# Kernel optimization log

Hardware: AMD Instinct MI355X
Metric: run time of the kernel (lower is better)

Reference implementation:

```python
import jax, jax.numpy as jnp
import numpy as np

D_IN = 1024
D_SAE = 16 * D_IN  # 16384
K = 32
BATCH = 8192


def setup_inputs() -> dict:
    key = jax.random.key(0)
    k0, k1, k2 = jax.random.split(key, 3)
    x = jax.random.normal(k0, (BATCH, D_IN), dtype=jnp.float32)
    # kaiming_uniform_ (fan_in, relu): bound = sqrt(6 / fan_in)
    b_enc_w = float(np.sqrt(6.0 / D_IN))
    b_dec_w = float(np.sqrt(6.0 / D_SAE))
    W_enc = jax.random.uniform(k1, (D_IN, D_SAE), minval=-b_enc_w, maxval=b_enc_w, dtype=jnp.float32)
    W_dec = jax.random.uniform(k2, (D_SAE, D_IN), minval=-b_dec_w, maxval=b_dec_w, dtype=jnp.float32)
    b_enc = jnp.zeros((D_SAE,), dtype=jnp.float32)
    b_dec = jnp.zeros((D_IN,), dtype=jnp.float32)
    return {"x": x, "W_enc": W_enc, "b_enc": b_enc, "W_dec": W_dec, "b_dec": b_dec}


def _top_k_sparse(pre_acts, k):
    # keep only top-k entries per row; equivalent to pre_acts * scatter-mask
    vals, idx = jax.lax.top_k(pre_acts, k)            # [B, k]
    rows = jnp.arange(pre_acts.shape[0])[:, None]      # [B, 1]
    return jnp.zeros_like(pre_acts).at[rows, idx].set(vals)


def reference(x, W_enc, b_enc, W_dec, b_dec):
    pre_acts = jax.nn.relu(x @ W_enc + b_enc)          # [B, d_sae]
    h_sparse = _top_k_sparse(pre_acts, K)              # [B, d_sae], k nonzeros/row
    x_hat = h_sparse @ W_dec + b_dec                   # [B, d_in]
    recon_loss = jnp.mean((x_hat - x) ** 2)
    l0 = jnp.mean(jnp.sum((h_sparse > 0).astype(jnp.float32), axis=-1))
    return x_hat, h_sparse, recon_loss, l0
```

## Files before the change

kernel.cpp:

```cpp
#include <hip/hip_runtime.h>

#define M_ 8192
#define N_ 16384
#define K_ 1024
#define TOPK 32
#define CCAP 512
#define NCAND 64
#define NX_ 8388608
#define NH_ 134217728
#define THRESH 3.0f
#define MARGIN 0.01f

typedef _Float16 f16;
typedef _Float16 f16x4 __attribute__((ext_vector_type(4)));
typedef _Float16 f16x8 __attribute__((ext_vector_type(8)));
typedef float f32x4 __attribute__((ext_vector_type(4)));

#define WT16_OFF ((size_t)0)
#define WT32_OFF ((size_t)32<<20)
#define XH_OFF   ((size_t)96<<20)
#define CIDX_OFF ((size_t)112<<20)
#define CVAL_OFF ((size_t)128<<20)
#define CCNT_OFF ((size_t)144<<20)
#define FIDX_OFF ((size_t)145<<20)
#define FCNT_OFF ((size_t)147<<20)
#define LIDX_OFF ((size_t)148<<20)
#define LVAL_OFF ((size_t)149<<20)
#define ACC_OFF  ((size_t)150<<20)

__global__ __launch_bounds__(256) void sae_cast_x(const float* __restrict__ x, f16* __restrict__ xh) {
    int i = (blockIdx.x * 256 + threadIdx.x) * 4;
    float4 v = *(const float4*)(x + i);
    f16x4 hv = {(f16)v.x, (f16)v.y, (f16)v.z, (f16)v.w};
    *(f16x4*)(xh + i) = hv;
}

__global__ __launch_bounds__(256) void sae_split_w(const float* __restrict__ W,
                                                   f16* __restrict__ bh, float* __restrict__ b32) {
    __shared__ float s32[64][65];
    const int n0 = blockIdx.x * 64, k0 = blockIdx.y * 64;
    const int t = threadIdx.x;
#pragma unroll
    for (int it = 0; it < 16; ++it) {
        int idx = t + 256 * it;
        int kl = idx >> 6, nl = idx & 63;
        s32[kl][nl] = W[(k0 + kl) * N_ + n0 + nl];
    }
    __syncthreads();
#pragma unroll
    for (int it = 0; it < 16; ++it) {
        int idx = t + 256 * it;
        int nl = idx >> 6, kl = idx & 63;
        float v = s32[kl][nl];
        bh[(n0 + nl) * K_ + k0 + kl] = (f16)v;
        b32[(n0 + nl) * K_ + k0 + kl] = v;
    }
}

__device__ __forceinline__ void gl_lds16(const void* g, void* l) {
    __builtin_amdgcn_global_load_lds((const __attribute__((address_space(1))) unsigned int*)g,
                                     (__attribute__((address_space(3))) unsigned int*)l, 16, 0, 0);
}

__global__ __launch_bounds__(256, 2) void sae_enc_gemm(const f16* __restrict__ A, const f16* __restrict__ B,
                                                       const float* __restrict__ benc, float* __restrict__ h,
                                                       int* __restrict__ cidx, float* __restrict__ cval,
                                                       int* __restrict__ ccnt) {
    __shared__ f16 sA[128 * 64];
    __shared__ f16 sB[128 * 64];
    const int t = threadIdx.x;
    const int lane = t & 63, w = t >> 6;
    const int wm = w >> 1, wn = w & 1;
    const int flat = blockIdx.x;
    const int xcd = flat & 7, pos = flat >> 3;
    const int bm = (((xcd << 3) + (pos & 7)) << 7);
    const int bn = ((pos >> 3) << 7);
    const int ar = lane & 15, kq4 = lane >> 4;
    f32x4 acc[4][4] = {};

    for (int kt = 0; kt < K_; kt += 64) {
        __syncthreads();
#pragma unroll
        for (int i = 0; i < 4; ++i) {
            int s16 = w * 64 + i * 256 + lane;
            int r = s16 >> 3, sc = s16 & 7;
            int c = sc ^ (r & 7);
            int gA = (bm + r) * K_ + kt + c * 8;
            int gB = (bn + r) * K_ + kt + c * 8;
            int ldsOff = (w * 64 + i * 256) * 8;
            gl_lds16(A + gA, sA + ldsOff);
            gl_lds16(B + gB, sB + ldsOff);
        }
        __syncthreads();
#pragma unroll
        for (int ks = 0; ks < 2; ++ks) {
            f16x8 fa[4], fb[4];
            const int cc = ks * 4 + kq4;
#pragma unroll
            for (int i = 0; i < 4; ++i) {
                int rA = wm * 64 + i * 16 + ar;
                fa[i] = *(const f16x8*)(sA + rA * 64 + ((cc ^ (rA & 7)) * 8));
                int rB = wn * 64 + i * 16 + ar;
                fb[i] = *(const f16x8*)(sB + rB * 64 + ((cc ^ (rB & 7)) * 8));
            }
#pragma unroll
            for (int i = 0; i < 4; ++i)
#pragma unroll
                for (int j = 0; j < 4; ++j)
                    acc[i][j] = __builtin_amdgcn_mfma_f32_16x16x32_f16(fa[i], fb[j], acc[i][j], 0, 0, 0);
        }
    }
    const int colb = bn + wn * 64 + ar;
    const int rq = (lane >> 4) * 4;
#pragma unroll
    for (int j = 0; j < 4; ++j) {
        int col = colb + j * 16;
        float bj = benc[col];
#pragma unroll
        for (int i = 0; i < 4; ++i) {
            int r0 = bm + wm * 64 + i * 16 + rq;
#pragma unroll
            for (int r = 0; r < 4; ++r) {
                float v = acc[i][j][r] + bj;
                if (v > THRESH) {
                    int row = r0 + r;
                    int slot = atomicAdd(&ccnt[row], 1);
                    if (slot < CCAP) { cidx[row * CCAP + slot] = col; cval[row * CCAP + slot] = v; }
                }
            }
        }
    }
    const f32x4 z4 = {0.f, 0.f, 0.f, 0.f};
#pragma unroll
    for (int z = 0; z < 16; ++z) {
        int idx = t + 256 * z;
        int row = idx >> 5, c4 = idx & 31;
        __builtin_nontemporal_store(z4, (f32x4*)(h + (long long)(bm + row) * N_ + bn + c4 * 4));
    }
}

__global__ __launch_bounds__(256) void sae_sel1(const int* __restrict__ cidx, const float* __restrict__ cval,
                                                const int* __restrict__ ccnt, int* __restrict__ fidx,
                                                int* __restrict__ fcnt) {
    const int row = blockIdx.x, t = threadIdx.x;
    int cnt = ccnt[row]; if (cnt > CCAP) cnt = CCAP;
    __shared__ float sv[CCAP];
    __shared__ int si[CCAP];
    __shared__ float sred[256];
    __shared__ int s_fc;
    for (int i = t; i < CCAP; i += 256) {
        sv[i] = (i < cnt) ? cval[row * CCAP + i] : -1e30f;
        si[i] = (i < cnt) ? cidx[row * CCAP + i] : 0;
    }
    if (t == 0) s_fc = 0;
    __syncthreads();
    float vmin = 1e30f;
    for (int i = t; i < cnt; i += 256) {
        float v = sv[i];
        int cgt = 0;
        for (int o = 0; o < cnt; ++o) cgt += (sv[o] > v);
        if (cgt < TOPK && v < vmin) vmin = v;
    }
    sred[t] = vmin;
    __syncthreads();
#pragma unroll
    for (int d = 128; d; d >>= 1) {
        if (t < d) sred[t] = fminf(sred[t], sred[t + d]);
        __syncthreads();
    }
    const float cutoff = sred[0] - MARGIN;
    for (int i = t; i < cnt; i += 256) {
        if (sv[i] > cutoff) {
            int s = atomicAdd(&s_fc, 1);
            if (s < NCAND) fidx[row * NCAND + s] = si[i];
        }
    }
    __syncthreads();
    if (t == 0) fcnt[row] = s_fc < NCAND ? s_fc : NCAND;
}

__global__ __launch_bounds__(64) void sae_npsel(const float* __restrict__ x, const float* __restrict__ Wt,
                                                const float* __restrict__ benc,
                                                const int* __restrict__ fidx, const int* __restrict__ fcnt,
                                                float* __restrict__ h, int* __restrict__ lidx,
                                                float* __restrict__ lval, unsigned int* __restrict__ l0cnt) {
    const int row = blockIdx.x, t = threadIdx.x;
    __shared__ float sx[1024];
    __shared__ float sW[NCAND][65];
    __shared__ double sv[NCAND];
    __shared__ int sj[NCAND];
    const int cnt = fcnt[row];
    const float* xr = x + (long long)row * K_;
#pragma unroll
    for (int i = 0; i < 4; ++i)
        *(float4*)(sx + t * 4 + i * 256) = *(const float4*)(xr + t * 4 + i * 256);
    const int myj = (t < cnt) ? fidx[row * NCAND + t] : 0x7FFFFFFF;
    sj[t] = myj;
    if (t < TOPK) { lidx[row * TOPK + t] = 0; lval[row * TOPK + t] = 0.f; }
    __syncthreads();

    double a0 = 0.0, a1 = 0.0, a2 = 0.0, a3 = 0.0;
    for (int k0 = 0; k0 < K_; k0 += 64) {
        for (int c = 0; c < cnt; ++c)
            sW[c][t] = Wt[(long long)sj[c] * K_ + k0 + t];
        __syncthreads();
        if (t < cnt) {
#pragma unroll
            for (int kk = 0; kk < 64; kk += 4) {
                a0 = fma((double)sx[k0 + kk + 0], (double)sW[t][kk + 0], a0);
                a1 = fma((double)sx[k0 + kk + 1], (double)sW[t][kk + 1], a1);
                a2 = fma((double)sx[k0 + kk + 2], (double)sW[t][kk + 2], a2);
                a3 = fma((double)sx[k0 + kk + 3], (double)sW[t][kk + 3], a3);
            }
        }
        __syncthreads();
    }
    const double acc = (a0 + a1) + (a2 + a3);
    double pre = -1.0e300;
    if (t < cnt) {
        pre = acc + (double)benc[myj];
        pre = pre > 0.0 ? pre : 0.0;
    }
    sv[t] = pre;
    __syncthreads();
    int l0loc = 0;
    if (t < cnt) {
        const double mv = sv[t];
        int rank = 0;
        for (int o = 0; o < cnt; ++o) {
            double ov = sv[o];
            if (ov > mv || (ov == mv && sj[o] < myj)) ++rank;
        }
        if (rank < TOPK) {
            float mvf = (float)mv;
            h[(long long)row * N_ + myj] = mvf;
            lidx[row * TOPK + rank] = myj;
            lval[row * TOPK + rank] = mvf;
            if (mvf > 0.f) l0loc = 1;
        }
    }
    unsigned long long ballot = __ballot(l0loc);
    if (t == 0) atomicAdd(l0cnt, (unsigned int)__popcll(ballot));
}

__global__ __launch_bounds__(256) void sae_dec(const float* __restrict__ x, const float* __restrict__ Wd,
                                               const float* __restrict__ bd, const int* __restrict__ lidx,
                                               const float* __restrict__ lval, float* __restrict__ xhat,
                                               double* __restrict__ lossacc) {
    const int row = blockIdx.x, t = threadIdx.x;
    __shared__ int si[32];
    __shared__ float sv[32];
    __shared__ float swsum[4];
    if (t < 32) {
        si[t] = lidx[row * TOPK + t];
        sv[t] = lval[row * TOPK + t];
    }
    __syncthreads();
    const int c = t * 4;
    float4 a = *(const float4*)(bd + c);
#pragma unroll 8
    for (int j = 0; j < 32; ++j) {
        float s = sv[j];
        float4 wv = *(const float4*)(Wd + si[j] * K_ + c);
        a.x += s * wv.x; a.y += s * wv.y; a.z += s * wv.z; a.w += s * wv.w;
    }
    *(float4*)(xhat + row * K_ + c) = a;
    float4 xv = *(const float4*)(x + row * K_ + c);
    float dx = a.x - xv.x, dy = a.y - xv.y, dz = a.z - xv.z, dw = a.w - xv.w;
    float se = dx * dx + dy * dy + dz * dz + dw * dw;
#pragma unroll
    for (int d = 32; d; d >>= 1) se += __shfl_down(se, d);
    if ((t & 63) == 0) swsum[t >> 6] = se;
    __syncthreads();
    if (t == 0) {
        float tot = swsum[0] + swsum[1] + swsum[2] + swsum[3];
        atomicAdd(lossacc, (double)tot);
    }
}

__global__ void sae_fin(const double* __restrict__ lossacc, const unsigned int* __restrict__ l0cnt,
                        float* __restrict__ tail) {
    tail[0] = (float)(lossacc[0] / (double)((long long)M_ * K_));
    tail[1] = (float)((double)l0cnt[0] / (double)M_);
}

extern "C" void kernel_launch(void* const* d_in, const int* in_sizes, int n_in,
                              void* d_out, int out_size, void* d_ws, size_t ws_size,
                              hipStream_t stream) {
    (void)in_sizes; (void)n_in; (void)out_size; (void)ws_size;
    const float* x = (const float*)d_in[0];
    const float* Wenc = (const float*)d_in[1];
    const float* benc = (const float*)d_in[2];
    const float* Wdec = (const float*)d_in[3];
    const float* bdec = (const float*)d_in[4];
    float* out = (float*)d_out;
    char* ws = (char*)d_ws;

    f16* wt16 = (f16*)(ws + WT16_OFF);
    float* wt32 = (float*)(ws + WT32_OFF);
    f16* xh = (f16*)(ws + XH_OFF);
    int* cidx = (int*)(ws + CIDX_OFF);
    float* cval = (float*)(ws + CVAL_OFF);
    int* ccnt = (int*)(ws + CCNT_OFF);
    int* fidx = (int*)(ws + FIDX_OFF);
    int* fcnt = (int*)(ws + FCNT_OFF);
    int* lidx = (int*)(ws + LIDX_OFF);
    float* lval = (float*)(ws + LVAL_OFF);
    double* lossacc = (double*)(ws + ACC_OFF);
    unsigned int* l0cnt = (unsigned int*)(ws + ACC_OFF + 8);

    hipMemsetAsync(ws + CCNT_OFF, 0, M_ * 4, stream);
    hipMemsetAsync(ws + ACC_OFF, 0, 16, stream);

    sae_cast_x<<<NX_ / 1024, 256, 0, stream>>>(x, xh);
    sae_split_w<<<dim3(N_ / 64, K_ / 64), 256, 0, stream>>>(Wenc, wt16, wt32);
    sae_enc_gemm<<<8192, 256, 0, stream>>>(xh, wt16, benc, out + NX_, cidx, cval, ccnt);
    sae_sel1<<<M_, 256, 0, stream>>>(cidx, cval, ccnt, fidx, fcnt);
    sae_npsel<<<M_, 64, 0, stream>>>(x, wt32, benc, fidx, fcnt, out + NX_, lidx, lval, l0cnt);
    sae_dec<<<M_, 256, 0, stream>>>(x, Wdec, bdec, lidx, lval, out, lossacc);
    sae_fin<<<1, 1, 0, stream>>>(lossacc, l0cnt, out + NX_ + NH_);
}
```

Before: 1.427 ms.

## Enlarge encoder GEMM tile to 256x256 with double-buffered async LDS prefetch

The encoder GEMM now uses 256x256 block tiles with 512 threads (8 waves, each computing 128x64), split into 32-wide K sub-tiles. It double-buffers shared memory so the global-to-LDS loads for the next K pair are issued while MFMAs run on the current buffer, synchronising with vmcnt waits and raw barriers instead of two __syncthreads per step. Wave priority is raised around the MFMA block. The goal is to cut global traffic per FLOP and hide load latency, at the cost of 64KB of LDS, more registers per thread and lower occupancy.

```diff
diff --git a/kernel.cpp b/kernel.cpp
--- a/kernel.cpp
+++ b/kernel.cpp
@@ -10,6 +10,11 @@
 #define NH_ 134217728
 #define THRESH 3.0f
 #define MARGIN 0.01f
+
+#define BM 256
+#define BN 256
+#define BKT 32
+#define NPAIR (K_ / (2 * BKT))
 
 typedef _Float16 f16;
 typedef _Float16 f16x4 __attribute__((ext_vector_type(4)));
@@ -62,66 +67,88 @@
                                      (__attribute__((address_space(3))) unsigned int*)l, 16, 0, 0);
 }
 
-__global__ __launch_bounds__(256, 2) void sae_enc_gemm(const f16* __restrict__ A, const f16* __restrict__ B,
+__global__ __launch_bounds__(512, 2) void sae_enc_gemm(const f16* __restrict__ A, const f16* __restrict__ B,
                                                        const float* __restrict__ benc, float* __restrict__ h,
                                                        int* __restrict__ cidx, float* __restrict__ cval,
                                                        int* __restrict__ ccnt) {
-    __shared__ f16 sA[128 * 64];
-    __shared__ f16 sB[128 * 64];
+    __shared__ __align__(16) f16 sm[2][2][2][8192];
     const int t = threadIdx.x;
     const int lane = t & 63, w = t >> 6;
-    const int wm = w >> 1, wn = w & 1;
+    const int wm = w >> 2, wn = w & 3;
     const int flat = blockIdx.x;
     const int xcd = flat & 7, pos = flat >> 3;
-    const int bm = (((xcd << 3) + (pos & 7)) << 7);
-    const int bn = ((pos >> 3) << 7);
-    const int ar = lane & 15, kq4 = lane >> 4;
-    f32x4 acc[4][4] = {};
-
-    for (int kt = 0; kt < K_; kt += 64) {
-        __syncthreads();
-#pragma unroll
-        for (int i = 0; i < 4; ++i) {
-            int s16 = w * 64 + i * 256 + lane;
-            int r = s16 >> 3, sc = s16 & 7;
-            int c = sc ^ (r & 7);
-            int gA = (bm + r) * K_ + kt + c * 8;
-            int gB = (bn + r) * K_ + kt + c * 8;
-            int ldsOff = (w * 64 + i * 256) * 8;
-            gl_lds16(A + gA, sA + ldsOff);
-            gl_lds16(B + gB, sB + ldsOff);
-        }
-        __syncthreads();
-#pragma unroll
-        for (int ks = 0; ks < 2; ++ks) {
-            f16x8 fa[4], fb[4];
-            const int cc = ks * 4 + kq4;
-#pragma unroll
-            for (int i = 0; i < 4; ++i) {
-                int rA = wm * 64 + i * 16 + ar;
-                fa[i] = *(const f16x8*)(sA + rA * 64 + ((cc ^ (rA & 7)) * 8));
-                int rB = wn * 64 + i * 16 + ar;
-                fb[i] = *(const f16x8*)(sB + rB * 64 + ((cc ^ (rB & 7)) * 8));
-            }
-#pragma unroll
-            for (int i = 0; i < 4; ++i)
-#pragma unroll
-                for (int j = 0; j < 4; ++j)
-                    acc[i][j] = __builtin_amdgcn_mfma_f32_16x16x32_f16(fa[i], fb[j], acc[i][j], 0, 0, 0);
-        }
-    }
-    const int colb = bn + wn * 64 + ar;
-    const int rq = (lane >> 4) * 4;
-#pragma unroll
-    for (int j = 0; j < 4; ++j) {
-        int col = colb + j * 16;
-        float bj = benc[col];
-#pragma unroll
-        for (int i = 0; i < 4; ++i) {
-            int r0 = bm + wm * 64 + i * 16 + rq;
+    const int bm = (xcd * 4 + (pos & 3)) * BM;
+    const int bn = (pos >> 2) * BN;
+    const int lr = lane & 15, kq = lane >> 4;
+
+    const int r_h = t >> 2, sc = t & 3;
+    const int cch = sc ^ ((r_h >> 1) & 3);
+    const int wuni = w * 512;
+
+    f32x4 acc[8][4] = {};
+
+#pragma unroll
+    for (int tt = 0; tt < 2; ++tt) {
+        const int kt = tt * BKT;
+        gl_lds16(A + (size_t)(bm + r_h) * K_ + kt + cch * 8,       &sm[0][tt][0][0]    + wuni);
+        gl_lds16(A + (size_t)(bm + 128 + r_h) * K_ + kt + cch * 8, &sm[0][tt][0][4096] + wuni);
+        gl_lds16(B + (size_t)(bn + r_h) * K_ + kt + cch * 8,       &sm[0][tt][1][0]    + wuni);
+        gl_lds16(B + (size_t)(bn + 128 + r_h) * K_ + kt + cch * 8, &sm[0][tt][1][4096] + wuni);
+    }
+    asm volatile("s_waitcnt vmcnt(4)" ::: "memory");
+    __builtin_amdgcn_s_barrier();
+
+#pragma unroll 1
+    for (int i = 0; i < NPAIR; ++i) {
+        const int buf = i & 1, nbuf = buf ^ 1;
+        const bool haveNext = (i + 1) < NPAIR;
+#pragma unroll
+        for (int sub = 0; sub < 2; ++sub) {
+            if (haveNext) {
+                const int kt = (i + 1) * 64 + sub * BKT;
+                gl_lds16(A + (size_t)(bm + r_h) * K_ + kt + cch * 8,       &sm[nbuf][sub][0][0]    + wuni);
+                gl_lds16(A + (size_t)(bm + 128 + r_h) * K_ + kt + cch * 8, &sm[nbuf][sub][0][4096] + wuni);
+                gl_lds16(B + (size_t)(bn + r_h) * K_ + kt + cch * 8,       &sm[nbuf][sub][1][0]    + wuni);
+                gl_lds16(B + (size_t)(bn + 128 + r_h) * K_ + kt + cch * 8, &sm[nbuf][sub][1][4096] + wuni);
+            }
+            f16x8 fa[8], fb[4];
+#pragma unroll
+            for (int m = 0; m < 8; ++m) {
+                const int ra = m * 16 + lr;
+                fa[m] = *(const f16x8*)(&sm[buf][sub][0][0] + wm * 4096 + ra * 32 +
+                                        ((kq ^ ((ra >> 1) & 3)) * 8));
+            }
+#pragma unroll
+            for (int n = 0; n < 4; ++n) {
+                const int rb = (wn & 1) * 64 + n * 16 + lr;
+                fb[n] = *(const f16x8*)(&sm[buf][sub][1][0] + (wn >> 1) * 4096 + rb * 32 +
+                                        ((kq ^ ((rb >> 1) & 3)) * 8));
+            }
+            __builtin_amdgcn_s_setprio(1);
+#pragma unroll
+            for (int m = 0; m < 8; ++m)
+#pragma unroll
+                for (int n = 0; n < 4; ++n)
+                    acc[m][n] = __builtin_amdgcn_mfma_f32_16x16x32_f16(fa[m], fb[n], acc[m][n], 0, 0, 0);
+            __builtin_amdgcn_s_setprio(0);
+            if (!haveNext && sub == 0) asm volatile("s_waitcnt vmcnt(0)" ::: "memory");
+            else                       asm volatile("s_waitcnt vmcnt(4)" ::: "memory");
+            __builtin_amdgcn_s_barrier();
+        }
+    }
+
+    const int colb = bn + wn * 64 + lr;
+    const int rq = kq * 4;
+#pragma unroll
+    for (int n = 0; n < 4; ++n) {
+        const int col = colb + n * 16;
+        const float bj = benc[col];
+#pragma unroll
+        for (int m = 0; m < 8; ++m) {
+            const int r0 = bm + wm * 128 + m * 16 + rq;
 #pragma unroll
             for (int r = 0; r < 4; ++r) {
-                float v = acc[i][j][r] + bj;
+                float v = acc[m][n][r] + bj;
                 if (v > THRESH) {
                     int row = r0 + r;
                     int slot = atomicAdd(&ccnt[row], 1);
@@ -132,10 +159,10 @@
     }
     const f32x4 z4 = {0.f, 0.f, 0.f, 0.f};
 #pragma unroll
-    for (int z = 0; z < 16; ++z) {
-        int idx = t + 256 * z;
-        int row = idx >> 5, c4 = idx & 31;
-        __builtin_nontemporal_store(z4, (f32x4*)(h + (long long)(bm + row) * N_ + bn + c4 * 4));
+    for (int z = 0; z < 32; ++z) {
+        int idx = t + 512 * z;
+        int row = idx >> 6, c4 = idx & 63;
+        __builtin_nontemporal_store(z4, (f32x4*)(h + (size_t)(bm + row) * N_ + bn + c4 * 4));
     }
 }
 
@@ -314,7 +341,7 @@
 
     sae_cast_x<<<NX_ / 1024, 256, 0, stream>>>(x, xh);
     sae_split_w<<<dim3(N_ / 64, K_ / 64), 256, 0, stream>>>(Wenc, wt16, wt32);
-    sae_enc_gemm<<<8192, 256, 0, stream>>>(xh, wt16, benc, out + NX_, cidx, cval, ccnt);
+    sae_enc_gemm<<<(M_ / BM) * (N_ / BN), 512, 0, stream>>>(xh, wt16, benc, out + NX_, cidx, cval, ccnt);
     sae_sel1<<<M_, 256, 0, stream>>>(cidx, cval, ccnt, fidx, fcnt);
     sae_npsel<<<M_, 64, 0, stream>>>(x, wt32, benc, fidx, fcnt, out + NX_, lidx, lval, l0cnt);
     sae_dec<<<M_, 256, 0, stream>>>(x, Wdec, bdec, lidx, lval, out, lossacc);
```

New measurement: 1.547 ms. +8.4%, slower.
